# Performance work log

Hardware: AMD Instinct MI355X
Metric: run time of the kernel (lower is better)

The kernel has to match this reference:

```python
import jax, jax.numpy as jnp
import numpy as np

N = 100000      # nodes
E = 1200000     # edges (avg degree ~12)
F_IN = 64       # input feature dim
HID = 64        # hidden_channels
OUT = 64        # out_channels


def setup_inputs() -> dict:
    key = jax.random.key(0)
    ks = jax.random.split(key, 9)
    s_in = 1.0 / np.sqrt(F_IN)
    s_h = 1.0 / np.sqrt(HID)
    inp = {
        "x": jax.random.normal(ks[0], (N, F_IN), dtype=jnp.float32),
        "edge_index": jax.random.randint(ks[1], (2, E), 0, N, dtype=jnp.int64),
        # conv_in: lin_l (with bias) applied to aggregated msgs, lin_r (no bias) to self
        "Wl_in": jax.random.normal(ks[2], (HID, F_IN), dtype=jnp.float32) * s_in,
        "bl_in": jnp.zeros((HID,), dtype=jnp.float32),
        "Wr_in": jax.random.normal(ks[3], (HID, F_IN), dtype=jnp.float32) * s_in,
        # conv_med (shared across the 2 middle applications)
        "Wl_med": jax.random.normal(ks[4], (HID, HID), dtype=jnp.float32) * s_h,
        "bl_med": jnp.zeros((HID,), dtype=jnp.float32),
        "Wr_med": jax.random.normal(ks[5], (HID, HID), dtype=jnp.float32) * s_h,
        # conv_out
        "Wl_out": jax.random.normal(ks[6], (OUT, HID), dtype=jnp.float32) * s_h,
        "bl_out": jnp.zeros((OUT,), dtype=jnp.float32),
        "Wr_out": jax.random.normal(ks[7], (OUT, HID), dtype=jnp.float32) * s_h,
    }
    return inp


def reference(x, edge_index, Wl_in, bl_in, Wr_in, Wl_med, bl_med, Wr_med,
              Wl_out, bl_out, Wr_out):
    src = edge_index[0]
    dst = edge_index[1]
    n = x.shape[0]

    def sage(h, Wl, bl, Wr):
        # sum-aggregate neighbor messages h_j into each destination node i
        agg = jax.ops.segment_sum(h[src], dst, num_segments=n)  # [N, F]
        return agg @ Wl.T + bl + h @ Wr.T

    # eval mode: dropout is identity
    h = jnp.tanh(sage(x, Wl_in, bl_in, Wr_in))
    for _ in range(2):  # conv_med applied twice with shared weights
        h = jnp.tanh(sage(h, Wl_med, bl_med, Wr_med))
    return sage(h, Wl_out, bl_out, Wr_out)
```

## Files before the change

### kernel.cpp

```cpp
#include <hip/hip_runtime.h>
#include <cstdint>

#define F 64
#define TILE1 8192
#define MAXFB 1024
#define SCAN_BLK 1024

typedef short bf16x8 __attribute__((ext_vector_type(8)));
typedef float f32x4  __attribute__((ext_vector_type(4)));

__device__ __forceinline__ unsigned short f2b(float f) {
    unsigned u = __float_as_uint(f);
    unsigned r = u + 0x7fffu + ((u >> 16) & 1u);
    return (unsigned short)(r >> 16);
}
__device__ __forceinline__ void add8(float* a, uint4 u) {
    const unsigned* p = (const unsigned*)&u;
#pragma unroll
    for (int i = 0; i < 4; ++i) {
        a[2 * i + 0] += __uint_as_float(p[i] << 16);
        a[2 * i + 1] += __uint_as_float(p[i] & 0xffff0000u);
    }
}

__global__ __launch_bounds__(256) void hist_kernel(
    const int* __restrict__ dst, int* __restrict__ binMat,
    int E, int NB1, int nf) {
    __shared__ int h[MAXFB];
    int t = threadIdx.x;
    for (int i = t; i < nf; i += 256) h[i] = 0;
    __syncthreads();
    int base = blockIdx.x * TILE1;
    int end = min(base + TILE1, E);
    const int4* d4 = (const int4*)dst;
    int n4 = (end - base) >> 2;
    int b4 = base >> 2;
    for (int k = t; k < n4; k += 256) {
        int4 v = d4[b4 + k];
        atomicAdd(&h[v.x >> 7], 1);
        atomicAdd(&h[v.y >> 7], 1);
        atomicAdd(&h[v.z >> 7], 1);
        atomicAdd(&h[v.w >> 7], 1);
    }
    __syncthreads();
    for (int i = t; i < nf; i += 256) binMat[i * NB1 + blockIdx.x] = h[i];
}

__global__ __launch_bounds__(SCAN_BLK) void scan_blocks_kernel(
    int* __restrict__ a, int* __restrict__ blockSums, int len) {
    __shared__ int sh[SCAN_BLK];
    int t = threadIdx.x;
    int i = blockIdx.x * SCAN_BLK + t;
    int v = (i < len) ? a[i] : 0;
    sh[t] = v;
    __syncthreads();
    for (int off = 1; off < SCAN_BLK; off <<= 1) {
        int add = (t >= off) ? sh[t - off] : 0;
        __syncthreads();
        sh[t] += add;
        __syncthreads();
    }
    int incl = sh[t];
    if (i < len) a[i] = incl - v;
    if (t == SCAN_BLK - 1) blockSums[blockIdx.x] = incl;
}

__global__ __launch_bounds__(SCAN_BLK) void scan_sums_kernel(
    int* __restrict__ blockSums, int nb) {
    __shared__ int sh[SCAN_BLK];
    int t = threadIdx.x;
    int v = (t < nb) ? blockSums[t] : 0;
    sh[t] = v;
    __syncthreads();
    for (int off = 1; off < SCAN_BLK; off <<= 1) {
        int add = (t >= off) ? sh[t - off] : 0;
        __syncthreads();
        sh[t] += add;
        __syncthreads();
    }
    if (t < nb) blockSums[t] = sh[t] - v;
}

__global__ __launch_bounds__(256) void scan_add_kernel(
    int* __restrict__ a, const int* __restrict__ blockSums, int len) {
    int i = blockIdx.x * 256 + threadIdx.x;
    if (i < len) a[i] += blockSums[i >> 10];
}

__global__ __launch_bounds__(256) void scatter_kernel(
    const int* __restrict__ src, const int* __restrict__ dst,
    const int* __restrict__ binMat, unsigned* __restrict__ stage2,
    int E, int NB1, int nf) {
    __shared__ int cur[MAXFB];
    int t = threadIdx.x;
    for (int i = t; i < nf; i += 256) cur[i] = binMat[i * NB1 + blockIdx.x];
    __syncthreads();
    int base = blockIdx.x * TILE1;
    int end = min(base + TILE1, E);
    const int4* s4 = (const int4*)src;
    const int4* d4 = (const int4*)dst;
    int n4 = (end - base) >> 2;
    int b4 = base >> 2;
    for (int k = t; k < n4; k += 256) {
        int4 s = s4[b4 + k];
        int4 d = d4[b4 + k];
        int p0 = atomicAdd(&cur[d.x >> 7], 1);
        int p1 = atomicAdd(&cur[d.y >> 7], 1);
        int p2 = atomicAdd(&cur[d.z >> 7], 1);
        int p3 = atomicAdd(&cur[d.w >> 7], 1);
        stage2[p0] = ((unsigned)(d.x & 127) << 17) | (unsigned)s.x;
        stage2[p1] = ((unsigned)(d.y & 127) << 17) | (unsigned)s.y;
        stage2[p2] = ((unsigned)(d.z & 127) << 17) | (unsigned)s.z;
        stage2[p3] = ((unsigned)(d.w & 127) << 17) | (unsigned)s.w;
    }
}

__global__ __launch_bounds__(256) void phase2_kernel(
    const unsigned* __restrict__ stage2, const int* __restrict__ binMat,
    int* __restrict__ csrSrc, int* __restrict__ rowStart,
    int E, int NB1, int nf) {
    __shared__ int cnt[128];
    __shared__ int pre[129];
    __shared__ int cur[128];
    int b = blockIdx.x;
    int t = threadIdx.x;
    int s = binMat[b * NB1];
    int e2 = (b + 1 < nf) ? binMat[(b + 1) * NB1] : E;
    if (t < 128) cnt[t] = 0;
    __syncthreads();
    for (int i = s + t; i < e2; i += 256)
        atomicAdd(&cnt[(stage2[i] >> 17) & 127], 1);
    __syncthreads();
    if (t < 128) pre[t + 1] = cnt[t];
    if (t == 0) pre[0] = 0;
    __syncthreads();
    for (int off = 1; off < 128; off <<= 1) {
        int v = 0;
        if (t < 128 && (t + 1) > off) v = pre[t + 1 - off];
        __syncthreads();
        if (t < 128 && (t + 1) > off) pre[t + 1] += v;
        __syncthreads();
    }
    if (t < 128) cur[t] = pre[t];
    if (t < 129) rowStart[b * 128 + t] = s + pre[t];
    __syncthreads();
    for (int i = s + t; i < e2; i += 256) {
        unsigned w = stage2[i];
        int pos = atomicAdd(&cur[(w >> 17) & 127], 1);
        csrSrc[s + pos] = (int)(w & 0x1FFFFu);
    }
}

__global__ __launch_bounds__(256) void prep_kernel(
    const float* __restrict__ Wl0, const float* __restrict__ Wr0,
    const float* __restrict__ Wl1, const float* __restrict__ Wr1,
    const float* __restrict__ Wl2, const float* __restrict__ Wr2,
    ushort* __restrict__ wbuf,
    const float* __restrict__ x, ushort* __restrict__ xb, int nElem) {
    int b = blockIdx.x;
    int t = threadIdx.x;
    if (b < 12) {
        int g = b * 256 + t;
        int set = g >> 10;
        int fl = g & 1023;
        int f = fl >> 6;
        int l = fl & 63;
        int s = f >> 2;
        int ot = f & 3;
        const float* Wl = (set == 0) ? Wl0 : (set == 1) ? Wl1 : Wl2;
        const float* Wr = (set == 0) ? Wr0 : (set == 1) ? Wr1 : Wr2;
        int o = ot * 16 + (l & 15);
        int k0 = s * 32 + (l >> 4) * 8;
        unsigned d[4];
#pragma unroll
        for (int p = 0; p < 4; ++p) {
            int ka = k0 + 2 * p, kb = k0 + 2 * p + 1;
            float va = (ka < 64) ? Wl[o * 64 + ka] : Wr[o * 64 + (ka - 64)];
            float vb = (kb < 64) ? Wl[o * 64 + kb] : Wr[o * 64 + (kb - 64)];
            d[p] = (unsigned)f2b(va) | ((unsigned)f2b(vb) << 16);
        }
        ((uint4*)wbuf)[g] = make_uint4(d[0], d[1], d[2], d[3]);
    } else {
        int i = (b - 12) * 256 + t;
        int n4 = nElem >> 2;
        if (i < n4) {
            float4 v = ((const float4*)x)[i];
            uint2 o;
            o.x = (unsigned)f2b(v.x) | ((unsigned)f2b(v.y) << 16);
            o.y = (unsigned)f2b(v.z) | ((unsigned)f2b(v.w) << 16);
            ((uint2*)xb)[i] = o;
        }
    }
}

__global__ __launch_bounds__(256, 4) void fused_layer(
    const ushort* __restrict__ hb, const int* __restrict__ rowStart,
    const int* __restrict__ csrSrc, const ushort* __restrict__ wbuf,
    const float* __restrict__ bl, void* __restrict__ out, int n, int flags) {
    __shared__ __align__(16) ushort smem[128 * 72];

    int t = threadIdx.x;
    int node0b = blockIdx.x * 128;
    const uint4* h16 = (const uint4*)hb;

    {
        int c = t & 7;
        int nlb = t >> 3;
#pragma unroll 1
        for (int r = 0; r < 4; ++r) {
            int nl = r * 32 + nlb;
            int node = node0b + nl;
            float a[8] = {0.f, 0.f, 0.f, 0.f, 0.f, 0.f, 0.f, 0.f};
            int e = rowStart[node];
            int end = rowStart[node + 1];
            for (; e + 3 < end; e += 4) {
                int s0 = csrSrc[e + 0];
                int s1 = csrSrc[e + 1];
                int s2 = csrSrc[e + 2];
                int s3 = csrSrc[e + 3];
                uint4 u0 = h16[(size_t)s0 * 8 + c];
                uint4 u1 = h16[(size_t)s1 * 8 + c];
                uint4 u2 = h16[(size_t)s2 * 8 + c];
                uint4 u3 = h16[(size_t)s3 * 8 + c];
                add8(a, u0); add8(a, u1); add8(a, u2); add8(a, u3);
            }
            for (; e < end; ++e) {
                uint4 u0 = h16[(size_t)csrSrc[e] * 8 + c];
                add8(a, u0);
            }
            unsigned d[4];
#pragma unroll
            for (int p = 0; p < 4; ++p)
                d[p] = (unsigned)f2b(a[2 * p]) | ((unsigned)f2b(a[2 * p + 1]) << 16);
            *(uint4*)(smem + nl * 72 + c * 8) = make_uint4(d[0], d[1], d[2], d[3]);
        }
    }
    __syncthreads();

    int w = t >> 6;
    int l = t & 63;
    int quad = l >> 4;
    int lo = l & 15;

    f32x4 acc[2][4];
#pragma unroll
    for (int ot = 0; ot < 4; ++ot) {
        float bv = bl[ot * 16 + lo];
        f32x4 bvv = {bv, bv, bv, bv};
        acc[0][ot] = bvv;
        acc[1][ot] = bvv;
    }

#pragma unroll
    for (int s = 0; s < 4; ++s) {
        bf16x8 A[2];
#pragma unroll
        for (int mt = 0; mt < 2; ++mt) {
            if (s < 2) {
                int nl = w * 32 + mt * 16 + lo;
                A[mt] = *(const bf16x8*)(smem + nl * 72 + s * 32 + quad * 8);
            } else {
                size_t node = (size_t)node0b + w * 32 + mt * 16 + lo;
                A[mt] = *(const bf16x8*)(hb + node * 64 + (s & 1) * 32 + quad * 8);
            }
        }
#pragma unroll
        for (int ot = 0; ot < 4; ++ot) {
            bf16x8 B = *(const bf16x8*)(wbuf + (((s * 4 + ot) * 64) + l) * 8);
#pragma unroll
            for (int mt = 0; mt < 2; ++mt)
                acc[mt][ot] = __builtin_amdgcn_mfma_f32_16x16x32_bf16(
                    A[mt], B, acc[mt][ot], 0, 0, 0);
        }
    }
    __syncthreads();

    float* outT = (float*)smem;
    int whalf = w >> 1;
    int wrow = (w & 1) * 32;

#pragma unroll
    for (int half = 0; half < 2; ++half) {
        if (whalf == half) {
#pragma unroll
            for (int mt = 0; mt < 2; ++mt) {
#pragma unroll
                for (int ot = 0; ot < 4; ++ot) {
                    f32x4 v = acc[mt][ot];
                    if (flags & 1) {
                        v[0] = tanhf(v[0]); v[1] = tanhf(v[1]);
                        v[2] = tanhf(v[2]); v[3] = tanhf(v[3]);
                    }
                    int row = wrow + mt * 16 + quad * 4;
                    int col = ot * 16 + lo;
#pragma unroll
                    for (int r = 0; r < 4; ++r)
                        outT[(row + r) * 68 + col] = v[r];
                }
            }
        }
        __syncthreads();
        int hr = t >> 2;
        int node = node0b + half * 64 + hr;
        if (node < n) {
            const float* srcp = &outT[hr * 68 + (t & 3) * 16];
            if (flags & 2) {
                uint4* o8 = (uint4*)out;
#pragma unroll
                for (int q = 0; q < 2; ++q) {
                    unsigned dd[4];
#pragma unroll
                    for (int p = 0; p < 4; ++p) {
                        float va = srcp[q * 8 + 2 * p];
                        float vb = srcp[q * 8 + 2 * p + 1];
                        dd[p] = (unsigned)f2b(va) | ((unsigned)f2b(vb) << 16);
                    }
                    o8[(size_t)node * 8 + (t & 3) * 2 + q] =
                        make_uint4(dd[0], dd[1], dd[2], dd[3]);
                }
            } else {
                float4* o16 = (float4*)out;
#pragma unroll
                for (int q = 0; q < 4; ++q) {
                    float4 v = *(const float4*)(srcp + q * 4);
                    o16[(size_t)node * 16 + (t & 3) * 4 + q] = v;
                }
            }
        }
        if (half == 0) __syncthreads();
    }
}

extern "C" void kernel_launch(void* const* d_in, const int* in_sizes, int n_in,
                              void* d_out, int out_size, void* d_ws, size_t ws_size,
                              hipStream_t stream) {
    const float* x      = (const float*)d_in[0];
    const int*   edges  = (const int*)d_in[1];
    const float* Wl_in  = (const float*)d_in[2];
    const float* bl_in  = (const float*)d_in[3];
    const float* Wr_in  = (const float*)d_in[4];
    const float* Wl_med = (const float*)d_in[5];
    const float* bl_med = (const float*)d_in[6];
    const float* Wr_med = (const float*)d_in[7];
    const float* Wl_out = (const float*)d_in[8];
    const float* bl_out = (const float*)d_in[9];
    const float* Wr_out = (const float*)d_in[10];

    const int N = in_sizes[0] / F;
    const int E = in_sizes[1] / 2;
    const int* src = edges;
    const int* dst = edges + E;

    const int nf  = (N + 127) >> 7;
    const int NB1 = (E + TILE1 - 1) / TILE1;
    const int NR  = nf * 128;
    const int scanLen = nf * NB1;
    const int nbScan = (scanLen + SCAN_BLK - 1) / SCAN_BLK;

    ushort*  wbuf      = (ushort*)d_ws;
    ushort*  xb        = wbuf + 3 * 8192;
    ushort*  hAb       = xb + (size_t)NR * F;
    ushort*  hBb       = hAb + (size_t)NR * F;
    int*     rowStart  = (int*)(hBb + (size_t)NR * F);
    int*     blockSums = rowStart + NR + 2;
    int*     binMat    = blockSums + SCAN_BLK;
    unsigned* stage2   = (unsigned*)(binMat + scanLen);
    int*     csrSrc    = (int*)(stage2 + E);

    const int prep_blocks = 12 + (N * F / 4 + 255) / 256;

    prep_kernel<<<prep_blocks, 256, 0, stream>>>(Wl_in, Wr_in, Wl_med, Wr_med,
                                                 Wl_out, Wr_out, wbuf, x, xb, N * F);

    hist_kernel<<<NB1, 256, 0, stream>>>(dst, binMat, E, NB1, nf);
    scan_blocks_kernel<<<nbScan, SCAN_BLK, 0, stream>>>(binMat, blockSums, scanLen);
    scan_sums_kernel<<<1, SCAN_BLK, 0, stream>>>(blockSums, nbScan);
    scan_add_kernel<<<(scanLen + 255) / 256, 256, 0, stream>>>(binMat, blockSums, scanLen);
    scatter_kernel<<<NB1, 256, 0, stream>>>(src, dst, binMat, stage2, E, NB1, nf);
    phase2_kernel<<<nf, 256, 0, stream>>>(stage2, binMat, csrSrc, rowStart, E, NB1, nf);

    fused_layer<<<nf, 256, 0, stream>>>(xb,  rowStart, csrSrc, wbuf,         bl_in,  hAb,   N, 3);
    fused_layer<<<nf, 256, 0, stream>>>(hAb, rowStart, csrSrc, wbuf + 8192,  bl_med, hBb,   N, 3);
    fused_layer<<<nf, 256, 0, stream>>>(hBb, rowStart, csrSrc, wbuf + 8192,  bl_med, hAb,   N, 3);
    fused_layer<<<nf, 256, 0, stream>>>(hAb, rowStart, csrSrc, wbuf + 16384, bl_out, d_out, N, 0);
}
```

Measured before the change: 297.0 us.

## Replace multi-kernel CSR build with single cooperative kernel using per-node global atomics

Merges weight/feature conversion, destination histogram, prefix scan and edge scatter into one cooperative kernel with grid-wide syncs, replacing seven separate launches. The two-level bucketed sort, which used LDS atomics, is replaced by direct per-node global atomic counting and scattering. This saves launch overhead and the intermediate staging pass. In exchange it relies on many contended global atomics and random writes, and neighbor order within a row becomes nondeterministic.

```diff
diff --git a/kernel.cpp b/kernel.cpp
--- a/kernel.cpp
+++ b/kernel.cpp
@@ -1,10 +1,12 @@
 #include <hip/hip_runtime.h>
+#include <hip/hip_cooperative_groups.h>
 #include <cstdint>
 
+namespace cg = cooperative_groups;
+
 #define F 64
-#define TILE1 8192
-#define MAXFB 1024
-#define SCAN_BLK 1024
+#define COOP_BLOCKS 256
+#define COOP_THREADS 1024
 
 typedef short bf16x8 __attribute__((ext_vector_type(8)));
 typedef float f32x4  __attribute__((ext_vector_type(4)));
@@ -23,144 +25,26 @@
     }
 }
 
-__global__ __launch_bounds__(256) void hist_kernel(
-    const int* __restrict__ dst, int* __restrict__ binMat,
-    int E, int NB1, int nf) {
-    __shared__ int h[MAXFB];
-    int t = threadIdx.x;
-    for (int i = t; i < nf; i += 256) h[i] = 0;
-    __syncthreads();
-    int base = blockIdx.x * TILE1;
-    int end = min(base + TILE1, E);
-    const int4* d4 = (const int4*)dst;
-    int n4 = (end - base) >> 2;
-    int b4 = base >> 2;
-    for (int k = t; k < n4; k += 256) {
-        int4 v = d4[b4 + k];
-        atomicAdd(&h[v.x >> 7], 1);
-        atomicAdd(&h[v.y >> 7], 1);
-        atomicAdd(&h[v.z >> 7], 1);
-        atomicAdd(&h[v.w >> 7], 1);
-    }
-    __syncthreads();
-    for (int i = t; i < nf; i += 256) binMat[i * NB1 + blockIdx.x] = h[i];
-}
-
-__global__ __launch_bounds__(SCAN_BLK) void scan_blocks_kernel(
-    int* __restrict__ a, int* __restrict__ blockSums, int len) {
-    __shared__ int sh[SCAN_BLK];
-    int t = threadIdx.x;
-    int i = blockIdx.x * SCAN_BLK + t;
-    int v = (i < len) ? a[i] : 0;
-    sh[t] = v;
-    __syncthreads();
-    for (int off = 1; off < SCAN_BLK; off <<= 1) {
-        int add = (t >= off) ? sh[t - off] : 0;
-        __syncthreads();
-        sh[t] += add;
-        __syncthreads();
-    }
-    int incl = sh[t];
-    if (i < len) a[i] = incl - v;
-    if (t == SCAN_BLK - 1) blockSums[blockIdx.x] = incl;
-}
-
-__global__ __launch_bounds__(SCAN_BLK) void scan_sums_kernel(
-    int* __restrict__ blockSums, int nb) {
-    __shared__ int sh[SCAN_BLK];
-    int t = threadIdx.x;
-    int v = (t < nb) ? blockSums[t] : 0;
-    sh[t] = v;
-    __syncthreads();
-    for (int off = 1; off < SCAN_BLK; off <<= 1) {
-        int add = (t >= off) ? sh[t - off] : 0;
-        __syncthreads();
-        sh[t] += add;
-        __syncthreads();
-    }
-    if (t < nb) blockSums[t] = sh[t] - v;
-}
-
-__global__ __launch_bounds__(256) void scan_add_kernel(
-    int* __restrict__ a, const int* __restrict__ blockSums, int len) {
-    int i = blockIdx.x * 256 + threadIdx.x;
-    if (i < len) a[i] += blockSums[i >> 10];
-}
-
-__global__ __launch_bounds__(256) void scatter_kernel(
-    const int* __restrict__ src, const int* __restrict__ dst,
-    const int* __restrict__ binMat, unsigned* __restrict__ stage2,
-    int E, int NB1, int nf) {
-    __shared__ int cur[MAXFB];
-    int t = threadIdx.x;
-    for (int i = t; i < nf; i += 256) cur[i] = binMat[i * NB1 + blockIdx.x];
-    __syncthreads();
-    int base = blockIdx.x * TILE1;
-    int end = min(base + TILE1, E);
-    const int4* s4 = (const int4*)src;
-    const int4* d4 = (const int4*)dst;
-    int n4 = (end - base) >> 2;
-    int b4 = base >> 2;
-    for (int k = t; k < n4; k += 256) {
-        int4 s = s4[b4 + k];
-        int4 d = d4[b4 + k];
-        int p0 = atomicAdd(&cur[d.x >> 7], 1);
-        int p1 = atomicAdd(&cur[d.y >> 7], 1);
-        int p2 = atomicAdd(&cur[d.z >> 7], 1);
-        int p3 = atomicAdd(&cur[d.w >> 7], 1);
-        stage2[p0] = ((unsigned)(d.x & 127) << 17) | (unsigned)s.x;
-        stage2[p1] = ((unsigned)(d.y & 127) << 17) | (unsigned)s.y;
-        stage2[p2] = ((unsigned)(d.z & 127) << 17) | (unsigned)s.z;
-        stage2[p3] = ((unsigned)(d.w & 127) << 17) | (unsigned)s.w;
-    }
-}
-
-__global__ __launch_bounds__(256) void phase2_kernel(
-    const unsigned* __restrict__ stage2, const int* __restrict__ binMat,
-    int* __restrict__ csrSrc, int* __restrict__ rowStart,
-    int E, int NB1, int nf) {
-    __shared__ int cnt[128];
-    __shared__ int pre[129];
-    __shared__ int cur[128];
-    int b = blockIdx.x;
-    int t = threadIdx.x;
-    int s = binMat[b * NB1];
-    int e2 = (b + 1 < nf) ? binMat[(b + 1) * NB1] : E;
-    if (t < 128) cnt[t] = 0;
-    __syncthreads();
-    for (int i = s + t; i < e2; i += 256)
-        atomicAdd(&cnt[(stage2[i] >> 17) & 127], 1);
-    __syncthreads();
-    if (t < 128) pre[t + 1] = cnt[t];
-    if (t == 0) pre[0] = 0;
-    __syncthreads();
-    for (int off = 1; off < 128; off <<= 1) {
-        int v = 0;
-        if (t < 128 && (t + 1) > off) v = pre[t + 1 - off];
-        __syncthreads();
-        if (t < 128 && (t + 1) > off) pre[t + 1] += v;
-        __syncthreads();
-    }
-    if (t < 128) cur[t] = pre[t];
-    if (t < 129) rowStart[b * 128 + t] = s + pre[t];
-    __syncthreads();
-    for (int i = s + t; i < e2; i += 256) {
-        unsigned w = stage2[i];
-        int pos = atomicAdd(&cur[(w >> 17) & 127], 1);
-        csrSrc[s + pos] = (int)(w & 0x1FFFFu);
-    }
-}
-
-__global__ __launch_bounds__(256) void prep_kernel(
+__global__ __launch_bounds__(COOP_THREADS) void preprocess_coop(
     const float* __restrict__ Wl0, const float* __restrict__ Wr0,
     const float* __restrict__ Wl1, const float* __restrict__ Wr1,
     const float* __restrict__ Wl2, const float* __restrict__ Wr2,
     ushort* __restrict__ wbuf,
-    const float* __restrict__ x, ushort* __restrict__ xb, int nElem) {
-    int b = blockIdx.x;
-    int t = threadIdx.x;
-    if (b < 12) {
-        int g = b * 256 + t;
+    const float* __restrict__ x, ushort* __restrict__ xb,
+    const int* __restrict__ src, const int* __restrict__ dst,
+    int* __restrict__ rowStart, int* __restrict__ cur,
+    int* __restrict__ blockSums, int* __restrict__ csrSrc,
+    int E, int N, int NR) {
+    cg::grid_group grid = cg::this_grid();
+    __shared__ int sh[COOP_THREADS];
+
+    const int t = threadIdx.x;
+    const int b = blockIdx.x;
+    const int gid = b * COOP_THREADS + t;
+    const int GT = COOP_BLOCKS * COOP_THREADS;
+
+    if (gid < 3072) {
+        int g = gid;
         int set = g >> 10;
         int fl = g & 1023;
         int f = fl >> 6;
@@ -180,16 +64,86 @@
             d[p] = (unsigned)f2b(va) | ((unsigned)f2b(vb) << 16);
         }
         ((uint4*)wbuf)[g] = make_uint4(d[0], d[1], d[2], d[3]);
-    } else {
-        int i = (b - 12) * 256 + t;
-        int n4 = nElem >> 2;
-        if (i < n4) {
-            float4 v = ((const float4*)x)[i];
+    }
+    {
+        int n4 = (N * F) >> 2;
+        const float4* x4 = (const float4*)x;
+        for (int i = gid; i < n4; i += GT) {
+            float4 v = x4[i];
             uint2 o;
             o.x = (unsigned)f2b(v.x) | ((unsigned)f2b(v.y) << 16);
             o.y = (unsigned)f2b(v.z) | ((unsigned)f2b(v.w) << 16);
             ((uint2*)xb)[i] = o;
         }
+    }
+    for (int i = gid; i < N; i += GT) cur[i] = 0;
+    grid.sync();
+
+    {
+        const int4* d4 = (const int4*)dst;
+        int n4 = E >> 2;
+        for (int i = gid; i < n4; i += GT) {
+            int4 v = d4[i];
+            atomicAdd(&cur[v.x], 1);
+            atomicAdd(&cur[v.y], 1);
+            atomicAdd(&cur[v.z], 1);
+            atomicAdd(&cur[v.w], 1);
+        }
+        for (int i = (E & ~3) + gid; i < E; i += GT) atomicAdd(&cur[dst[i]], 1);
+    }
+    grid.sync();
+
+    int i3 = b * COOP_THREADS + t;
+    int v3 = (i3 < N) ? cur[i3] : 0;
+    sh[t] = v3;
+    __syncthreads();
+    for (int off = 1; off < COOP_THREADS; off <<= 1) {
+        int add = (t >= off) ? sh[t - off] : 0;
+        __syncthreads();
+        sh[t] += add;
+        __syncthreads();
+    }
+    int incl = sh[t];
+    if (t == COOP_THREADS - 1) blockSums[b] = incl;
+    grid.sync();
+
+    if (b == 0) {
+        int bv = (t < COOP_BLOCKS) ? blockSums[t] : 0;
+        sh[t] = bv;
+        __syncthreads();
+        for (int off = 1; off < COOP_BLOCKS; off <<= 1) {
+            int add = (t >= off) ? sh[t - off] : 0;
+            __syncthreads();
+            sh[t] += add;
+            __syncthreads();
+        }
+        if (t < COOP_BLOCKS) blockSums[t] = sh[t] - bv;
+    }
+    grid.sync();
+
+    {
+        int off0 = blockSums[b];
+        int excl = incl - v3 + off0;
+        if (i3 < N) { rowStart[i3] = excl; cur[i3] = excl; }
+        for (int j = gid; j <= NR; j += GT)
+            if (j >= N) rowStart[j] = E;
+    }
+    grid.sync();
+
+    {
+        const int4* s4 = (const int4*)src;
+        const int4* d4 = (const int4*)dst;
+        int n4 = E >> 2;
+        for (int i = gid; i < n4; i += GT) {
+            int4 sv = s4[i];
+            int4 dv = d4[i];
+            csrSrc[atomicAdd(&cur[dv.x], 1)] = sv.x;
+            csrSrc[atomicAdd(&cur[dv.y], 1)] = sv.y;
+            csrSrc[atomicAdd(&cur[dv.z], 1)] = sv.z;
+            csrSrc[atomicAdd(&cur[dv.w], 1)] = sv.w;
+        }
+        for (int i = (E & ~3) + gid; i < E; i += GT)
+            csrSrc[atomicAdd(&cur[dst[i]], 1)] = src[i];
     }
 }
 
@@ -348,36 +302,32 @@
 
     const int N = in_sizes[0] / F;
     const int E = in_sizes[1] / 2;
-    const int* src = edges;
-    const int* dst = edges + E;
-
-    const int nf  = (N + 127) >> 7;
-    const int NB1 = (E + TILE1 - 1) / TILE1;
-    const int NR  = nf * 128;
-    const int scanLen = nf * NB1;
-    const int nbScan = (scanLen + SCAN_BLK - 1) / SCAN_BLK;
+    const int* srcp = edges;
+    const int* dstp = edges + E;
+
+    const int nf = (N + 127) >> 7;
+    const int NR = nf * 128;
 
     ushort*  wbuf      = (ushort*)d_ws;
     ushort*  xb        = wbuf + 3 * 8192;
     ushort*  hAb       = xb + (size_t)NR * F;
     ushort*  hBb       = hAb + (size_t)NR * F;
     int*     rowStart  = (int*)(hBb + (size_t)NR * F);
-    int*     blockSums = rowStart + NR + 2;
-    int*     binMat    = blockSums + SCAN_BLK;
-    unsigned* stage2   = (unsigned*)(binMat + scanLen);
-    int*     csrSrc    = (int*)(stage2 + E);
-
-    const int prep_blocks = 12 + (N * F / 4 + 255) / 256;
-
-    prep_kernel<<<prep_blocks, 256, 0, stream>>>(Wl_in, Wr_in, Wl_med, Wr_med,
-                                                 Wl_out, Wr_out, wbuf, x, xb, N * F);
-
-    hist_kernel<<<NB1, 256, 0, stream>>>(dst, binMat, E, NB1, nf);
-    scan_blocks_kernel<<<nbScan, SCAN_BLK, 0, stream>>>(binMat, blockSums, scanLen);
-    scan_sums_kernel<<<1, SCAN_BLK, 0, stream>>>(blockSums, nbScan);
-    scan_add_kernel<<<(scanLen + 255) / 256, 256, 0, stream>>>(binMat, blockSums, scanLen);
-    scatter_kernel<<<NB1, 256, 0, stream>>>(src, dst, binMat, stage2, E, NB1, nf);
-    phase2_kernel<<<nf, 256, 0, stream>>>(stage2, binMat, csrSrc, rowStart, E, NB1, nf);
+    int*     cur       = rowStart + NR + 16;
+    int*     blockSums = cur + NR;
+    int*     csrSrc    = blockSums + 1024;
+
+    int Ei = E, Ni = N, NRi = NR;
+    void* args[] = {
+        (void*)&Wl_in, (void*)&Wr_in, (void*)&Wl_med, (void*)&Wr_med,
+        (void*)&Wl_out, (void*)&Wr_out, (void*)&wbuf,
+        (void*)&x, (void*)&xb,
+        (void*)&srcp, (void*)&dstp,
+        (void*)&rowStart, (void*)&cur, (void*)&blockSums, (void*)&csrSrc,
+        (void*)&Ei, (void*)&Ni, (void*)&NRi,
+    };
+    hipLaunchCooperativeKernel(preprocess_coop, dim3(COOP_BLOCKS),
+                               dim3(COOP_THREADS), args, 0u, stream);
 
     fused_layer<<<nf, 256, 0, stream>>>(xb,  rowStart, csrSrc, wbuf,         bl_in,  hAb,   N, 3);
     fused_layer<<<nf, 256, 0, stream>>>(hAb, rowStart, csrSrc, wbuf + 8192,  bl_med, hBb,   N, 3);
```

New measurement: 559.2 us. 88.3% more time.
